# Kernel optimization log

Measured on AMD Instinct MI355X. Metric: run time of the kernel, lower is better.

Reference implementation:

```python
import jax, jax.numpy as jnp
import numpy as np

# dims: L = 1 + H*W tokens (cls first), BT = B*T clips*frames
L, BT, D = 577, 128, 768
B, T = 16, 8
H = W = 24
CM = 192   # d_middle = D // REDUCTION(4)
CR = 48    # CM // rf_r(4)
K = 3      # rf_k and spatial kernel


def setup_inputs() -> dict:
    key = jax.random.key(0)
    ks = jax.random.split(key, 10)
    return {
        "x":      jax.random.normal(ks[0], (L, BT, D), jnp.float32),
        # tada_pre_proj: Linear(D -> CM)
        "w_pre":  jax.random.normal(ks[1], (D, CM), jnp.float32) * 0.02,
        "b_pre":  jnp.zeros((CM,), jnp.float32),
        # TAdaConv2dV2 base depthwise weight (1x3x3, groups=CM) and bias
        "w_base": jax.random.normal(ks[2], (K, K, 1, CM), jnp.float32) * 0.1,
        "b_conv": jnp.zeros((CM,), jnp.float32),
        # route function: global 1x1 branch, temporal conv a (CM->CR), temporal conv b (CR->CM, small init)
        "w_g":    jax.random.normal(ks[3], (CM, CM), jnp.float32) * 0.02,
        "b_g":    jnp.zeros((CM,), jnp.float32),
        "w_a":    jax.random.normal(ks[4], (K, CM, CR), jnp.float32) * 0.05,
        "b_a":    jnp.zeros((CR,), jnp.float32),
        "w_b":    jax.random.normal(ks[5], (K, CR, CM), jnp.float32) * 0.02,
        # tada_proj: Linear(CM -> D)
        "w_proj": jax.random.normal(ks[6], (CM, D), jnp.float32) * 0.02,
        "b_proj": jnp.zeros((D,), jnp.float32),
    }


def reference(x, w_pre, b_pre, w_base, b_conv, w_g, b_g, w_a, b_a, w_b, w_proj, b_proj):
    # --- tada_pre_proj ---
    h = x @ w_pre + b_pre                                   # [L, BT, CM]
    cls_tok, sp = h[:1], h[1:]                              # cls token bypasses the conv
    sp = sp.transpose(1, 0, 2).reshape(BT, H, W, CM)        # [BT, H, W, CM]

    # --- route function: per-frame, per-channel calibration alpha ---
    d = sp.reshape(B, T, H * W, CM).mean(axis=2)            # spatial avg pool -> [B, T, CM]
    g = d.mean(axis=1) @ w_g + b_g                          # global temporal descriptor [B, CM]
    a = jax.lax.conv_general_dilated(d + g[:, None, :], w_a, (1,), 'SAME',
                                     dimension_numbers=('NWC', 'WIO', 'NWC')) + b_a
    a = jax.nn.relu(a)                                      # [B, T, CR]
    alpha = jax.lax.conv_general_dilated(a, w_b, (1,), 'SAME',
                                         dimension_numbers=('NWC', 'WIO', 'NWC')) + 1.0  # [B, T, CM]

    # --- calibrated depthwise conv (cal_dim='cout') ---
    # conv2d(x, alpha * W_base) == alpha * conv2d(x, W_base) for depthwise cout calibration
    y = jax.lax.conv_general_dilated(sp, w_base, (1, 1), 'SAME',
                                     dimension_numbers=('NHWC', 'HWIO', 'NHWC'),
                                     feature_group_count=CM)
    y = y * alpha.reshape(BT, 1, 1, CM) + b_conv            # [BT, H, W, CM]
    y = y.reshape(BT, H * W, CM).transpose(1, 0, 2)         # [HW, BT, CM]
    out = jnp.concatenate([cls_tok, y], axis=0)             # [L, BT, CM]

    # --- QuickGELU + tada_proj ---
    out = out * jax.nn.sigmoid(1.702 * out)
    return out @ w_proj + b_proj                            # [L, BT, D]
```

## Files before the change

### kernel.cpp

```cpp
#include <hip/hip_runtime.h>

#define DEV __device__ __forceinline__

typedef short bf16x8 __attribute__((ext_vector_type(8)));
typedef float f32x4  __attribute__((ext_vector_type(4)));
typedef unsigned short ushort_t;


DEV unsigned short f2bf(float f) {
  unsigned u = __float_as_uint(f);
  unsigned r = (u + 0x7fffu + ((u >> 16) & 1u)) >> 16;
  return (unsigned short)r;
}

DEV unsigned cvt_pk_bf16(float a, float b) {
  unsigned r;
  asm("v_cvt_pk_bf16_f32 %0, %1, %2" : "=v"(r) : "v"(a), "v"(b));
  return r;
}

DEV float bf2f(unsigned short b) { return __uint_as_float((unsigned)b << 16); }

DEV float silu_g(float v) { return v / (1.f + __expf(-1.702f * v)); }

DEV void gload_lds16(const void* g, void* l) {
  __builtin_amdgcn_global_load_lds(
      (const __attribute__((address_space(1))) unsigned int*)g,
      (__attribute__((address_space(3))) unsigned int*)l, 16, 0, 0);
}

__global__ __launch_bounds__(256)
void prep_kernel(const float* __restrict__ w_pre, const float* __restrict__ w_proj,
                 short* __restrict__ w_preT, short* __restrict__ w_projT) {
  int i = blockIdx.x * 256 + threadIdx.x;
  if (i < 192 * 768) {
    int n = i / 768, k = i - n * 768;
    w_preT[i] = (short)f2bf(w_pre[k * 192 + n]);
    int n2 = i / 192, k2 = i - n2 * 192;
    w_projT[i] = (short)f2bf(w_proj[k2 * 768 + n2]);
  }
}

__global__ __launch_bounds__(512, 4)
void gemm1_kernel(const float* __restrict__ Af, const short* __restrict__ Bt,
                  const float* __restrict__ bias, ushort_t* __restrict__ C) {
  constexpr int BM = 128, BK = 64, KTOT = 768, NTOT = 192, NT = 12;
  __shared__ short As[2][BM * BK];
  __shared__ short Bs[2][192 * BK];

  const int tid  = threadIdx.x;
  const int wave = tid >> 6, lane = tid & 63;
  const int m0 = blockIdx.x * BM;
  const int wm = wave >> 2, wn = wave & 3;
  const int lr  = lane & 15;
  const int lk8 = lane >> 4;
  const int srow = lane >> 3;
  const int schunk = lane & 7;

  f32x4 acc[4][3] = {};
  float4 areg[2][2];

  auto loadA_f32 = [&](int kt) {
    #pragma unroll
    for (int s = 0; s < 2; ++s) {
      int id = tid + s * 512;
      int r = id >> 3, c = id & 7;
      int cg = c ^ (r & 7);
      const float* p = Af + (size_t)(m0 + r) * KTOT + kt + cg * 8;
      areg[s][0] = *(const float4*)p;
      areg[s][1] = *(const float4*)(p + 4);
    }
  };
  auto cvtStoreA = [&](int buf) {
    #pragma unroll
    for (int s = 0; s < 2; ++s) {
      int id = tid + s * 512;
      int r = id >> 3, c = id & 7;
      int4 w;
      w.x = (int)cvt_pk_bf16(areg[s][0].x, areg[s][0].y);
      w.y = (int)cvt_pk_bf16(areg[s][0].z, areg[s][0].w);
      w.z = (int)cvt_pk_bf16(areg[s][1].x, areg[s][1].y);
      w.w = (int)cvt_pk_bf16(areg[s][1].z, areg[s][1].w);
      *(int4*)&As[buf][r * 64 + c * 8] = w;
    }
  };
  auto stageB = [&](int kt, int buf) {
    #pragma unroll
    for (int j = 0; j < 3; ++j) {
      int rb8 = wave * 3 + j;
      int r = rb8 * 8 + srow;
      const short* src = Bt + (size_t)r * KTOT + kt + (schunk ^ srow) * 8;
      gload_lds16(src, (char*)Bs[buf] + rb8 * 1024);
    }
  };
  auto compute = [&](int buf) {
    #pragma unroll
    for (int ks = 0; ks < 2; ++ks) {
      int kc = ks * 4 + lk8;
      bf16x8 af[4], bfv[3];
      #pragma unroll
      for (int fm = 0; fm < 4; ++fm) {
        int row = wm * 64 + fm * 16 + lr;
        af[fm] = *(const bf16x8*)&As[buf][row * 64 + (kc ^ (row & 7)) * 8];
      }
      #pragma unroll
      for (int fn = 0; fn < 3; ++fn) {
        int row = wn * 48 + fn * 16 + lr;
        bfv[fn] = *(const bf16x8*)&Bs[buf][row * 64 + (kc ^ (row & 7)) * 8];
      }
      #pragma unroll
      for (int fm = 0; fm < 4; ++fm)
        #pragma unroll
        for (int fn = 0; fn < 3; ++fn)
          acc[fm][fn] = __builtin_amdgcn_mfma_f32_16x16x32_bf16(
              bfv[fn], af[fm], acc[fm][fn], 0, 0, 0);
    }
  };

  loadA_f32(0);
  cvtStoreA(0);
  stageB(0, 0);
  loadA_f32(BK);
  asm volatile("s_waitcnt vmcnt(4) lgkmcnt(0)" ::: "memory");
  __builtin_amdgcn_s_barrier();

  #pragma unroll
  for (int t = 0; t < NT; ++t) {
    const int cur = t & 1, nxt = cur ^ 1;
    if (t + 1 < NT) {
      stageB((t + 1) * BK, nxt);
      cvtStoreA(nxt);
      if (t + 2 < NT) loadA_f32((t + 2) * BK);
    }
    compute(cur);
    if (t + 1 < NT) {
      if (t + 2 < NT)
        asm volatile("s_waitcnt vmcnt(4) lgkmcnt(0)" ::: "memory");
      else
        asm volatile("s_waitcnt vmcnt(0) lgkmcnt(0)" ::: "memory");
      __builtin_amdgcn_s_barrier();
    }
  }

  const int cb = (lane >> 4) * 4;
  #pragma unroll
  for (int fm = 0; fm < 4; ++fm) {
    int row = m0 + wm * 64 + fm * 16 + lr;
    #pragma unroll
    for (int fn = 0; fn < 3; ++fn) {
      int col = wn * 48 + fn * 16 + cb;
      float4 bv = *(const float4*)(bias + col);
      int2 w;
      w.x = (int)cvt_pk_bf16(acc[fm][fn][0] + bv.x, acc[fm][fn][1] + bv.y);
      w.y = (int)cvt_pk_bf16(acc[fm][fn][2] + bv.z, acc[fm][fn][3] + bv.w);
      *(int2*)&C[(size_t)row * NTOT + col] = w;
    }
  }
}

__global__ __launch_bounds__(384)
void reduce_d_kernel(const ushort_t* __restrict__ h, float* __restrict__ d) {
  const int bt = blockIdx.x, tid = threadIdx.x;
  const int slice = tid / 24, c8 = tid % 24;
  __shared__ float part[16][192];
  float sum[8] = {};
  #pragma unroll 4
  for (int i = 0; i < 36; ++i) {
    int l = 1 + slice * 36 + i;
    bf16x8 v = *(const bf16x8*)&h[((size_t)l * 128 + bt) * 192 + c8 * 8];
    #pragma unroll
    for (int j = 0; j < 8; ++j) sum[j] += bf2f((unsigned short)v[j]);
  }
  #pragma unroll
  for (int j = 0; j < 8; ++j) part[slice][c8 * 8 + j] = sum[j];
  __syncthreads();
  if (tid < 192) {
    float s = 0.f;
    #pragma unroll
    for (int sl = 0; sl < 16; ++sl) s += part[sl][tid];
    d[bt * 192 + tid] = s * (1.f / 576.f);
  }
}

__global__ __launch_bounds__(256)
void small_path_kernel(const float* __restrict__ d,
                       const float* __restrict__ w_g, const float* __restrict__ b_g,
                       const float* __restrict__ w_a, const float* __restrict__ b_a,
                       const float* __restrict__ w_b,
                       float* __restrict__ alpha) {
  const int b = blockIdx.x, tid = threadIdx.x;
  __shared__ unsigned short wg_buf[36864];
  __shared__ unsigned short wa_buf[27648];
  __shared__ float e[8][192];
  __shared__ float md[192];
  __shared__ float a[8][48];

  #pragma unroll
  for (int it = 0; it < 36; ++it) {
    int i = tid + it * 256;
    float4 v = *(const float4*)(w_g + i * 4);
    int2 w;
    w.x = (int)cvt_pk_bf16(v.x, v.y);
    w.y = (int)cvt_pk_bf16(v.z, v.w);
    *(int2*)&wg_buf[i * 4] = w;
  }
  #pragma unroll
  for (int it = 0; it < 27; ++it) {
    int i = tid + it * 256;
    float4 v = *(const float4*)(w_a + i * 4);
    int2 w;
    w.x = (int)cvt_pk_bf16(v.x, v.y);
    w.y = (int)cvt_pk_bf16(v.z, v.w);
    *(int2*)&wa_buf[i * 4] = w;
  }
  for (int i = tid; i < 384; i += 256)
    *(float4*)((float*)e + i * 4) = *(const float4*)(d + (size_t)b * 1536 + i * 4);
  __syncthreads();

  if (tid < 192) {
    float m = 0.f;
    #pragma unroll
    for (int t = 0; t < 8; ++t) m += e[t][tid];
    md[tid] = m * 0.125f;
  }
  __syncthreads();

  if (tid < 192) {
    float accg = b_g[tid];
    #pragma unroll 8
    for (int k = 0; k < 192; ++k)
      accg += md[k] * bf2f(wg_buf[k * 192 + tid]);
    #pragma unroll
    for (int t = 0; t < 8; ++t) e[t][tid] += accg;
  }
  __syncthreads();

  #pragma unroll
  for (int it = 0; it < 27; ++it) {
    int i = tid + it * 256;
    float4 v = *(const float4*)(w_b + i * 4);
    int2 w;
    w.x = (int)cvt_pk_bf16(v.x, v.y);
    w.y = (int)cvt_pk_bf16(v.z, v.w);
    *(int2*)&wg_buf[i * 4] = w;
  }
  for (int o = tid; o < 384; o += 256) {
    int t = o / 48, r = o - t * 48;
    float acc = b_a[r];
    #pragma unroll
    for (int dt = 0; dt < 3; ++dt) {
      int tt = t + dt - 1;
      if ((unsigned)tt < 8u) {
        #pragma unroll 8
        for (int k = 0; k < 192; ++k)
          acc += e[tt][k] * bf2f(wa_buf[(dt * 192 + k) * 48 + r]);
      }
    }
    a[t][r] = fmaxf(acc, 0.f);
  }
  __syncthreads();

  if (tid < 192) {
    #pragma unroll
    for (int t = 0; t < 8; ++t) {
      float acc = 1.0f;
      #pragma unroll
      for (int dt = 0; dt < 3; ++dt) {
        int tt = t + dt - 1;
        if ((unsigned)tt < 8u) {
          #pragma unroll 8
          for (int r = 0; r < 48; ++r)
            acc += a[tt][r] * bf2f(wg_buf[(dt * 48 + r) * 192 + tid]);
        }
      }
      alpha[(size_t)(b * 8 + t) * 192 + tid] = acc;
    }
  }
}

__global__ __launch_bounds__(512, 2)
void fused_out_kernel(const ushort_t* __restrict__ h, const float* __restrict__ alpha,
                      const float* __restrict__ w_base, const float* __restrict__ b_conv,
                      const short* __restrict__ Bt, const float* __restrict__ bias,
                      float* __restrict__ out) {
  constexpr int KTOT = 192, NTOT = 768;
  __shared__ ushort_t Stile[128 * 192];
  __shared__ short    Btile[192 * 192];

  const int tid  = threadIdx.x;
  const int blk  = blockIdx.x;
  const int wave = tid >> 6, lane = tid & 63;
  const int wm = wave >> 2, wn = wave & 3;
  const int lr = lane & 15, lk8 = lane >> 4;

  const int row = tid >> 2;
  const int cg  = tid & 3;
  if (blk == 0) {
    #pragma unroll
    for (int j = 0; j < 6; ++j) {
      int c8 = cg + 4 * j;
      bf16x8 hv = *(const bf16x8*)&h[(size_t)row * 192 + c8 * 8];
      int4 pk;
      float v0 = silu_g(bf2f((ushort_t)hv[0])), v1 = silu_g(bf2f((ushort_t)hv[1]));
      float v2 = silu_g(bf2f((ushort_t)hv[2])), v3 = silu_g(bf2f((ushort_t)hv[3]));
      float v4 = silu_g(bf2f((ushort_t)hv[4])), v5 = silu_g(bf2f((ushort_t)hv[5]));
      float v6 = silu_g(bf2f((ushort_t)hv[6])), v7 = silu_g(bf2f((ushort_t)hv[7]));
      pk.x = (int)cvt_pk_bf16(v0, v1); pk.y = (int)cvt_pk_bf16(v2, v3);
      pk.z = (int)cvt_pk_bf16(v4, v5); pk.w = (int)cvt_pk_bf16(v6, v7);
      int chp = (c8 & ~7) | ((c8 & 7) ^ (row & 7));
      *(int4*)&Stile[row * 192 + chp * 8] = pk;
    }
  } else {
    const int p = blk - 1, hh = p / 24, ww = p - hh * 24;
    #pragma unroll
    for (int j = 0; j < 6; ++j) {
      int c8 = cg + 4 * j;
      int cbase = c8 * 8;
      float acc8[8] = {};
      #pragma unroll
      for (int dh = 0; dh < 3; ++dh) {
        int y = hh + dh - 1;
        if ((unsigned)y >= 24u) continue;
        #pragma unroll
        for (int dw = 0; dw < 3; ++dw) {
          int xx = ww + dw - 1;
          if ((unsigned)xx >= 24u) continue;
          bf16x8 hv = *(const bf16x8*)
              &h[((size_t)(1 + y * 24 + xx) * 128 + row) * 192 + cbase];
          const float* wp = w_base + (dh * 3 + dw) * 192 + cbase;
          float4 w0 = *(const float4*)wp, w1 = *(const float4*)(wp + 4);
          acc8[0] += bf2f((ushort_t)hv[0]) * w0.x;
          acc8[1] += bf2f((ushort_t)hv[1]) * w0.y;
          acc8[2] += bf2f((ushort_t)hv[2]) * w0.z;
          acc8[3] += bf2f((ushort_t)hv[3]) * w0.w;
          acc8[4] += bf2f((ushort_t)hv[4]) * w1.x;
          acc8[5] += bf2f((ushort_t)hv[5]) * w1.y;
          acc8[6] += bf2f((ushort_t)hv[6]) * w1.z;
          acc8[7] += bf2f((ushort_t)hv[7]) * w1.w;
        }
      }
      const float* ap = alpha + (size_t)row * 192 + cbase;
      float4 a0 = *(const float4*)ap, a1 = *(const float4*)(ap + 4);
      const float* bp = b_conv + cbase;
      float4 c0 = *(const float4*)bp, c1 = *(const float4*)(bp + 4);
      float v0 = silu_g(acc8[0] * a0.x + c0.x), v1 = silu_g(acc8[1] * a0.y + c0.y);
      float v2 = silu_g(acc8[2] * a0.z + c0.z), v3 = silu_g(acc8[3] * a0.w + c0.w);
      float v4 = silu_g(acc8[4] * a1.x + c1.x), v5 = silu_g(acc8[5] * a1.y + c1.y);
      float v6 = silu_g(acc8[6] * a1.z + c1.z), v7 = silu_g(acc8[7] * a1.w + c1.w);
      int4 pk;
      pk.x = (int)cvt_pk_bf16(v0, v1); pk.y = (int)cvt_pk_bf16(v2, v3);
      pk.z = (int)cvt_pk_bf16(v4, v5); pk.w = (int)cvt_pk_bf16(v6, v7);
      int chp = (c8 & ~7) | ((c8 & 7) ^ (row & 7));
      *(int4*)&Stile[row * 192 + chp * 8] = pk;
    }
  }

  #pragma unroll 1
  for (int nc = 0; nc < 4; ++nc) {
    const int n0 = nc * 192;
    __syncthreads();

    #pragma unroll
    for (int i = 0; i < 9; ++i) {
      int q = wave * 576 + i * 64 + lane;
      int brow = q / 24;
      int ch = q - brow * 24;
      int ach = (ch & ~7) | ((ch & 7) ^ (brow & 7));
      const short* src = Bt + (size_t)(n0 + brow) * KTOT + ach * 8;
      gload_lds16(src, (char*)Btile + (wave * 9 + i) * 1024);
    }
    asm volatile("s_waitcnt vmcnt(0)" ::: "memory");
    __builtin_amdgcn_s_barrier();

    f32x4 acc[4][3] = {};
    #pragma unroll
    for (int kt = 0; kt < 3; ++kt) {
      #pragma unroll
      for (int ks = 0; ks < 2; ++ks) {
        int kc = kt * 8 + ks * 4 + lk8;
        bf16x8 af[4], bfv[3];
        #pragma unroll
        for (int fm = 0; fm < 4; ++fm) {
          int sr = wm * 64 + fm * 16 + lr;
          int chp = (kc & ~7) | ((kc & 7) ^ (sr & 7));
          af[fm] = *(const bf16x8*)&Stile[sr * 192 + chp * 8];
        }
        #pragma unroll
        for (int fn = 0; fn < 3; ++fn) {
          int br = wn * 48 + fn * 16 + lr;
          int chp = (kc & ~7) | ((kc & 7) ^ (br & 7));
          bfv[fn] = *(const bf16x8*)&Btile[br * 192 + chp * 8];
        }
        #pragma unroll
        for (int fm = 0; fm < 4; ++fm)
          #pragma unroll
          for (int fn = 0; fn < 3; ++fn)
            acc[fm][fn] = __builtin_amdgcn_mfma_f32_16x16x32_bf16(
                bfv[fn], af[fm], acc[fm][fn], 0, 0, 0);
      }
    }

    const int cb = (lane >> 4) * 4;
    #pragma unroll
    for (int fm = 0; fm < 4; ++fm) {
      int orow = blk * 128 + wm * 64 + fm * 16 + lr;
      #pragma unroll
      for (int fn = 0; fn < 3; ++fn) {
        int col = n0 + wn * 48 + fn * 16 + cb;
        float4 bv = *(const float4*)(bias + col);
        f32x4 o;
        o[0] = acc[fm][fn][0] + bv.x;
        o[1] = acc[fm][fn][1] + bv.y;
        o[2] = acc[fm][fn][2] + bv.z;
        o[3] = acc[fm][fn][3] + bv.w;
        __builtin_nontemporal_store(o, (f32x4*)&out[(size_t)orow * NTOT + col]);
      }
    }
  }
}

extern "C" void kernel_launch(void* const* d_in, const int* in_sizes, int n_in,
                              void* d_out, int out_size, void* d_ws, size_t ws_size,
                              hipStream_t stream) {
  (void)in_sizes; (void)n_in; (void)out_size; (void)ws_size;
  const float* x      = (const float*)d_in[0];
  const float* w_pre  = (const float*)d_in[1];
  const float* b_pre  = (const float*)d_in[2];
  const float* w_base = (const float*)d_in[3];
  const float* b_conv = (const float*)d_in[4];
  const float* w_g    = (const float*)d_in[5];
  const float* b_g    = (const float*)d_in[6];
  const float* w_a    = (const float*)d_in[7];
  const float* b_a    = (const float*)d_in[8];
  const float* w_b    = (const float*)d_in[9];
  const float* w_proj = (const float*)d_in[10];
  const float* b_proj = (const float*)d_in[11];

  float* out = (float*)d_out;
  char* ws = (char*)d_ws;
  short* w_preT  = (short*)(ws);
  short* w_projT = (short*)(ws + 294912);
  float* dbuf    = (float*)(ws + 589824);
  float* alpha   = (float*)(ws + 688128);
  ushort_t* h    = (ushort_t*)(ws + 786432);

  prep_kernel<<<576, 256, 0, stream>>>(w_pre, w_proj, w_preT, w_projT);

  gemm1_kernel<<<577, 512, 0, stream>>>(x, w_preT, b_pre, h);

  reduce_d_kernel<<<128, 384, 0, stream>>>(h, dbuf);
  small_path_kernel<<<16, 256, 0, stream>>>(dbuf, w_g, b_g, w_a, b_a, w_b, alpha);

  fused_out_kernel<<<577, 512, 0, stream>>>(h, alpha, w_base, b_conv,
                                            w_projT, b_proj, out);
}
```

Before: 241.3 us.

## Split fused output kernel into half-row blocks and read projection weights from global

Measured after the change: 242.6 us. About the same (+0.5%).

```diff
diff --git a/kernel.cpp b/kernel.cpp
--- a/kernel.cpp
+++ b/kernel.cpp
@@ -278,43 +278,44 @@
   }
 }
 
-__global__ __launch_bounds__(512, 2)
+__global__ __launch_bounds__(512, 4)
 void fused_out_kernel(const ushort_t* __restrict__ h, const float* __restrict__ alpha,
                       const float* __restrict__ w_base, const float* __restrict__ b_conv,
                       const short* __restrict__ Bt, const float* __restrict__ bias,
                       float* __restrict__ out) {
-  constexpr int KTOT = 192, NTOT = 768;
-  __shared__ ushort_t Stile[128 * 192];
-  __shared__ short    Btile[192 * 192];
+  constexpr int NTOT = 768;
+  __shared__ ushort_t Stile[64 * 192];
 
   const int tid  = threadIdx.x;
-  const int blk  = blockIdx.x;
+  const int l    = blockIdx.x >> 1;
+  const int bt0  = (blockIdx.x & 1) * 64;
   const int wave = tid >> 6, lane = tid & 63;
   const int wm = wave >> 2, wn = wave & 3;
   const int lr = lane & 15, lk8 = lane >> 4;
 
-  const int row = tid >> 2;
-  const int cg  = tid & 3;
-  if (blk == 0) {
-    #pragma unroll
-    for (int j = 0; j < 6; ++j) {
-      int c8 = cg + 4 * j;
-      bf16x8 hv = *(const bf16x8*)&h[(size_t)row * 192 + c8 * 8];
-      int4 pk;
+  const int row = tid >> 3;
+  const int cg  = tid & 7;
+  const int bt  = bt0 + row;
+  if (l == 0) {
+    #pragma unroll
+    for (int j = 0; j < 3; ++j) {
+      int c8 = cg + 8 * j;
+      bf16x8 hv = *(const bf16x8*)&h[(size_t)bt * 192 + c8 * 8];
       float v0 = silu_g(bf2f((ushort_t)hv[0])), v1 = silu_g(bf2f((ushort_t)hv[1]));
       float v2 = silu_g(bf2f((ushort_t)hv[2])), v3 = silu_g(bf2f((ushort_t)hv[3]));
       float v4 = silu_g(bf2f((ushort_t)hv[4])), v5 = silu_g(bf2f((ushort_t)hv[5]));
       float v6 = silu_g(bf2f((ushort_t)hv[6])), v7 = silu_g(bf2f((ushort_t)hv[7]));
+      int4 pk;
       pk.x = (int)cvt_pk_bf16(v0, v1); pk.y = (int)cvt_pk_bf16(v2, v3);
       pk.z = (int)cvt_pk_bf16(v4, v5); pk.w = (int)cvt_pk_bf16(v6, v7);
       int chp = (c8 & ~7) | ((c8 & 7) ^ (row & 7));
       *(int4*)&Stile[row * 192 + chp * 8] = pk;
     }
   } else {
-    const int p = blk - 1, hh = p / 24, ww = p - hh * 24;
-    #pragma unroll
-    for (int j = 0; j < 6; ++j) {
-      int c8 = cg + 4 * j;
+    const int p = l - 1, hh = p / 24, ww = p - hh * 24;
+    #pragma unroll
+    for (int j = 0; j < 3; ++j) {
+      int c8 = cg + 8 * j;
       int cbase = c8 * 8;
       float acc8[8] = {};
       #pragma unroll
@@ -326,7 +327,7 @@
           int xx = ww + dw - 1;
           if ((unsigned)xx >= 24u) continue;
           bf16x8 hv = *(const bf16x8*)
-              &h[((size_t)(1 + y * 24 + xx) * 128 + row) * 192 + cbase];
+              &h[((size_t)(1 + y * 24 + xx) * 128 + bt) * 192 + cbase];
           const float* wp = w_base + (dh * 3 + dw) * 192 + cbase;
           float4 w0 = *(const float4*)wp, w1 = *(const float4*)(wp + 4);
           acc8[0] += bf2f((ushort_t)hv[0]) * w0.x;
@@ -339,7 +340,7 @@
           acc8[7] += bf2f((ushort_t)hv[7]) * w1.w;
         }
       }
-      const float* ap = alpha + (size_t)row * 192 + cbase;
+      const float* ap = alpha + (size_t)bt * 192 + cbase;
       float4 a0 = *(const float4*)ap, a1 = *(const float4*)(ap + 4);
       const float* bp = b_conv + cbase;
       float4 c0 = *(const float4*)bp, c1 = *(const float4*)(bp + 4);
@@ -354,56 +355,42 @@
       *(int4*)&Stile[row * 192 + chp * 8] = pk;
     }
   }
-
+  __syncthreads();
+
+  bf16x8 areg[6][2];
+  #pragma unroll
+  for (int kt = 0; kt < 6; ++kt) {
+    #pragma unroll
+    for (int fm = 0; fm < 2; ++fm) {
+      int sr = wm * 32 + fm * 16 + lr;
+      int kc = kt * 4 + lk8;
+      int chp = (kc & ~7) | ((kc & 7) ^ (sr & 7));
+      areg[kt][fm] = *(const bf16x8*)&Stile[sr * 192 + chp * 8];
+    }
+  }
+
+  const int cb = (lane >> 4) * 4;
   #pragma unroll 1
   for (int nc = 0; nc < 4; ++nc) {
     const int n0 = nc * 192;
-    __syncthreads();
-
-    #pragma unroll
-    for (int i = 0; i < 9; ++i) {
-      int q = wave * 576 + i * 64 + lane;
-      int brow = q / 24;
-      int ch = q - brow * 24;
-      int ach = (ch & ~7) | ((ch & 7) ^ (brow & 7));
-      const short* src = Bt + (size_t)(n0 + brow) * KTOT + ach * 8;
-      gload_lds16(src, (char*)Btile + (wave * 9 + i) * 1024);
-    }
-    asm volatile("s_waitcnt vmcnt(0)" ::: "memory");
-    __builtin_amdgcn_s_barrier();
-
-    f32x4 acc[4][3] = {};
-    #pragma unroll
-    for (int kt = 0; kt < 3; ++kt) {
-      #pragma unroll
-      for (int ks = 0; ks < 2; ++ks) {
-        int kc = kt * 8 + ks * 4 + lk8;
-        bf16x8 af[4], bfv[3];
+    f32x4 acc[2][3] = {};
+    #pragma unroll
+    for (int kt = 0; kt < 6; ++kt) {
+      bf16x8 bfv[3];
+      #pragma unroll
+      for (int fn = 0; fn < 3; ++fn)
+        bfv[fn] = *(const bf16x8*)(Bt +
+            (size_t)(n0 + wn * 48 + fn * 16 + lr) * 192 + kt * 32 + lk8 * 8);
+      #pragma unroll
+      for (int fm = 0; fm < 2; ++fm)
         #pragma unroll
-        for (int fm = 0; fm < 4; ++fm) {
-          int sr = wm * 64 + fm * 16 + lr;
-          int chp = (kc & ~7) | ((kc & 7) ^ (sr & 7));
-          af[fm] = *(const bf16x8*)&Stile[sr * 192 + chp * 8];
-        }
-        #pragma unroll
-        for (int fn = 0; fn < 3; ++fn) {
-          int br = wn * 48 + fn * 16 + lr;
-          int chp = (kc & ~7) | ((kc & 7) ^ (br & 7));
-          bfv[fn] = *(const bf16x8*)&Btile[br * 192 + chp * 8];
-        }
-        #pragma unroll
-        for (int fm = 0; fm < 4; ++fm)
-          #pragma unroll
-          for (int fn = 0; fn < 3; ++fn)
-            acc[fm][fn] = __builtin_amdgcn_mfma_f32_16x16x32_bf16(
-                bfv[fn], af[fm], acc[fm][fn], 0, 0, 0);
-      }
-    }
-
-    const int cb = (lane >> 4) * 4;
-    #pragma unroll
-    for (int fm = 0; fm < 4; ++fm) {
-      int orow = blk * 128 + wm * 64 + fm * 16 + lr;
+        for (int fn = 0; fn < 3; ++fn)
+          acc[fm][fn] = __builtin_amdgcn_mfma_f32_16x16x32_bf16(
+              bfv[fn], areg[kt][fm], acc[fm][fn], 0, 0, 0);
+    }
+    #pragma unroll
+    for (int fm = 0; fm < 2; ++fm) {
+      int orow = l * 128 + bt0 + wm * 32 + fm * 16 + lr;
       #pragma unroll
       for (int fn = 0; fn < 3; ++fn) {
         int col = n0 + wn * 48 + fn * 16 + cb;
@@ -451,6 +438,6 @@
   reduce_d_kernel<<<128, 384, 0, stream>>>(h, dbuf);
   small_path_kernel<<<16, 256, 0, stream>>>(dbuf, w_g, b_g, w_a, b_a, w_b, alpha);
 
-  fused_out_kernel<<<577, 512, 0, stream>>>(h, alpha, w_base, b_conv,
-                                            w_projT, b_proj, out);
-}
+  fused_out_kernel<<<1154, 512, 0, stream>>>(h, alpha, w_base, b_conv,
+                                             w_projT, b_proj, out);
+}
```
